# Kernel tuning notes

Hardware: AMD Instinct MI355X
Metric: run time of the kernel (lower is better)

Reference implementation:

```python
import jax, jax.numpy as jnp
import numpy as np

D = 128   # input_dim / num vars
LEAKY_SLOPE = 0.01  # torch F.leaky_relu default


def setup_inputs() -> dict:
    key = jax.random.key(0)
    ks = jax.random.split(key, 7)
    h, o, b = 64, 2, 8192
    scale = 0.05  # keep activations in a sane range
    return {
        "x": jax.random.normal(ks[0], (b, D), jnp.float32),
        "w0": jax.random.normal(ks[1], (D, h, D), jnp.float32) * scale,
        "w1": jax.random.normal(ks[2], (D, h, h), jnp.float32) * scale,
        "w2": jax.random.normal(ks[3], (D, o, h), jnp.float32) * scale,
        "b0": jax.random.normal(ks[4], (D, h), jnp.float32) * scale,
        "b1": jax.random.normal(ks[5], (D, h), jnp.float32) * scale,
        "b2": jax.random.normal(ks[6], (D, o), jnp.float32) * scale,
    }


def reference(x, w0, w1, w2, b0, b1, b2):
    # adjacency: all-ones minus identity (variable t cannot see itself)
    adj = jnp.ones((D, D), x.dtype) - jnp.eye(D, dtype=x.dtype)  # [j? no: (i,j)] symmetric
    # layer 0: out[b,t,i] = sum_j w0[t,i,j] * adj[j,t] * x[b,j]
    # mask the per-variable weights once, then a single contraction (no (t,i,j,b) intermediate)
    w0m = w0 * adj.T[:, None, :]            # (t,i,j); adj symmetric so adj[j,t]==adj[t,j]
    h = jnp.einsum('tij,bj->bti', w0m, x) + b0
    h = jax.nn.leaky_relu(h, LEAKY_SLOPE)
    # layer 1: per-variable dense
    h = jnp.einsum('tij,btj->bti', w1, h) + b1
    h = jax.nn.leaky_relu(h, LEAKY_SLOPE)
    # layer 2 (output, no nonlinearity)
    out = jnp.einsum('tij,btj->bti', w2, h) + b2  # (b, D, output_dim)
    # torch version returns torch.unbind(out, 1); stacked array carries same values
    return out
```

## Files before the change

kernel.cpp:

```cpp
#include <hip/hip_runtime.h>


typedef __bf16 bf16_t;
typedef __bf16 bf16x8 __attribute__((ext_vector_type(8)));
typedef float  f32x4  __attribute__((ext_vector_type(4)));

#define LEAKY 0.01f

#define XB_OFF   0u
#define W0B_OFF  (2048u*1024u)
#define W1B_OFF  (4096u*1024u)

__global__ __launch_bounds__(256)
void brickify(const float* __restrict__ x,  const float* __restrict__ w0,
              const float* __restrict__ w1, unsigned char* __restrict__ ws)
{
    const int wid  = blockIdx.x * 4 + (threadIdx.x >> 6);
    const int lane = threadIdx.x & 63;
    const int lr = lane & 15, lq = lane >> 4;

    float v[8];
    if (wid < 2048) {
        int bt = wid >> 5, rem = wid & 31, nt = rem >> 2, ks = rem & 3;
        const float* s = x + (size_t)(bt*128 + nt*16 + lr) * 128 + ks*32 + lq*8;
        const float4 a = *(const float4*)s, b = *(const float4*)(s + 4);
        v[0]=a.x; v[1]=a.y; v[2]=a.z; v[3]=a.w;
        v[4]=b.x; v[5]=b.y; v[6]=b.z; v[7]=b.w;
    } else if (wid < 4096) {
        int u = wid - 2048, t = u >> 4, rem = u & 15, it = rem >> 2, ks = rem & 3;
        int k0 = ks*32 + lq*8;
        const float* s = w0 + (size_t)(t*64 + it*16 + lr) * 128 + k0;
        const float4 a = *(const float4*)s, b = *(const float4*)(s + 4);
        v[0]=a.x; v[1]=a.y; v[2]=a.z; v[3]=a.w;
        v[4]=b.x; v[5]=b.y; v[6]=b.z; v[7]=b.w;
        #pragma unroll
        for (int j = 0; j < 8; ++j) if (k0 + j == t) v[j] = 0.f;
    } else {
        int u = wid - 4096, t = u >> 3, rem = u & 7, it = rem >> 1, ks = rem & 1;
        const float* s = w1 + (size_t)(t*64 + it*16 + lr) * 64 + ks*32 + lq*8;
        const float4 a = *(const float4*)s, b = *(const float4*)(s + 4);
        v[0]=a.x; v[1]=a.y; v[2]=a.z; v[3]=a.w;
        v[4]=b.x; v[5]=b.y; v[6]=b.z; v[7]=b.w;
    }
    union { bf16_t h[8]; uint4 q; } pk;
    #pragma unroll
    for (int j = 0; j < 8; ++j) pk.h[j] = (bf16_t)v[j];
    ((uint4*)ws)[(size_t)wid * 64 + lane] = pk.q;
}

__global__ __launch_bounds__(512, 2)
void fused_mlp(const unsigned char* __restrict__ ws,
               const float* __restrict__ w2,
               const float* __restrict__ b0, const float* __restrict__ b1,
               const float* __restrict__ b2, float* __restrict__ out)
{
    __shared__ __align__(16) unsigned char hsm[16384];

    const int tid  = threadIdx.x;
    const int w    = tid >> 6;
    const int lane = tid & 63;
    const int lr = lane & 15, lq = lane >> 4;
    const int g  = blockIdx.x;
    const int t  = blockIdx.y;

    const unsigned char* w0p = ws + W0B_OFF + (size_t)t*16384 + lane*16;
    const unsigned char* w1p = ws + W1B_OFF + (size_t)t*8192  + lane*16;
    bf16x8 w0f[4][4], w1f[4][2];
    #pragma unroll
    for (int it = 0; it < 4; ++it)
        #pragma unroll
        for (int ks = 0; ks < 4; ++ks)
            w0f[it][ks] = *(const bf16x8*)(w0p + (it*4+ks)*1024);
    #pragma unroll
    for (int it = 0; it < 4; ++it)
        #pragma unroll
        for (int ks = 0; ks < 2; ++ks)
            w1f[it][ks] = *(const bf16x8*)(w1p + (it*2+ks)*1024);

    f32x4 w2v[2][4];
    #pragma unroll
    for (int o = 0; o < 2; ++o)
        #pragma unroll
        for (int it = 0; it < 4; ++it)
            w2v[o][it] = *(const f32x4*)(w2 + t*128 + o*64 + it*16 + lq*4);

    f32x4 b0q[4], b1q[4];
    #pragma unroll
    for (int it = 0; it < 4; ++it) {
        b0q[it] = *(const f32x4*)(b0 + t*64 + it*16 + lq*4);
        b1q[it] = *(const f32x4*)(b1 + t*64 + it*16 + lq*4);
    }
    const float2 b2v = *(const float2*)(b2 + t*2);

    const unsigned char* xp = ws + XB_OFF + lane*16;
    bf16x8 xf[4];
    #pragma unroll
    for (int ks = 0; ks < 4; ++ks)
        xf[ks] = *(const bf16x8*)(xp + (size_t)((g*8*8 + w)*4 + ks)*1024);

    const int wboff = ((lq >> 1) * 16 + lr) * 16 + (lq & 1) * 8;

    bf16x8 hf[2];
    f32x4  acc1[4];

    #pragma unroll
    for (int s = 0; s <= 8; ++s) {
        const int bt = g*8 + s;

        f32x4 acc0[4];
        if (s < 8) {
            #pragma unroll
            for (int it = 0; it < 4; ++it) acc0[it] = b0q[it];
            #pragma unroll
            for (int ks = 0; ks < 4; ++ks)
                #pragma unroll
                for (int it = 0; it < 4; ++it)
                    acc0[it] = __builtin_amdgcn_mfma_f32_16x16x32_bf16(
                                   w0f[it][ks], xf[ks], acc0[it], 0, 0, 0);
            if (s < 7) {
                #pragma unroll
                for (int ks = 0; ks < 4; ++ks)
                    xf[ks] = *(const bf16x8*)(xp + (size_t)(((bt+1)*8 + w)*4 + ks)*1024);
            }
        }

        if (s > 0) {
            #pragma unroll
            for (int it = 0; it < 4; ++it) acc1[it] = b1q[it];
            #pragma unroll
            for (int ks = 0; ks < 2; ++ks)
                #pragma unroll
                for (int it = 0; it < 4; ++it)
                    acc1[it] = __builtin_amdgcn_mfma_f32_16x16x32_bf16(
                                   w1f[it][ks], hf[ks], acc1[it], 0, 0, 0);
        }

        if (s < 8) {
            #pragma unroll
            for (int it = 0; it < 4; ++it) {
                union { bf16_t h[4]; unsigned long long u; } pk;
                #pragma unroll
                for (int r = 0; r < 4; ++r) {
                    float u = acc0[it][r];
                    pk.h[r] = (bf16_t)fmaxf(u, LEAKY * u);
                }
                int off = (w*2 + (it>>1)) * 1024 + (it&1) * 512 + wboff;
                *(unsigned long long*)(hsm + off) = pk.u;
            }
            #pragma unroll
            for (int ks = 0; ks < 2; ++ks)
                hf[ks] = *(const bf16x8*)(hsm + (w*2 + ks)*1024 + lane*16);
        }

        if (s > 0) {
            float p0 = 0.f, p1 = 0.f;
            #pragma unroll
            for (int it = 0; it < 4; ++it)
                #pragma unroll
                for (int r = 0; r < 4; ++r) {
                    float u = acc1[it][r];
                    u = fmaxf(u, LEAKY * u);
                    p0 = fmaf(w2v[0][it][r], u, p0);
                    p1 = fmaf(w2v[1][it][r], u, p1);
                }
            p0 += __shfl_xor(p0, 16); p0 += __shfl_xor(p0, 32);
            p1 += __shfl_xor(p1, 16); p1 += __shfl_xor(p1, 32);
            if (lq == 0) {
                int row = (bt - 1)*128 + w*16 + lr;
                float2 o2 = { p0 + b2v.x, p1 + b2v.y };
                *(float2*)(out + (size_t)row*256 + t*2) = o2;
            }
        }
    }
}

extern "C" void kernel_launch(void* const* d_in, const int* in_sizes, int n_in,
                              void* d_out, int out_size, void* d_ws, size_t ws_size,
                              hipStream_t stream) {
    const float* x  = (const float*)d_in[0];
    const float* w0 = (const float*)d_in[1];
    const float* w1 = (const float*)d_in[2];
    const float* w2 = (const float*)d_in[3];
    const float* b0 = (const float*)d_in[4];
    const float* b1 = (const float*)d_in[5];
    const float* b2 = (const float*)d_in[6];
    unsigned char* ws = (unsigned char*)d_ws;
    float* out = (float*)d_out;

    brickify<<<dim3(1280), dim3(256), 0, stream>>>(x, w0, w1, ws);
    fused_mlp<<<dim3(8, 128), dim3(512), 0, stream>>>(ws, w2, b0, b1, b2, out);
}
```

Baseline: 113.3 us.

## Shrink fused MLP blocks and cut register use to raise occupancy

Halves the fused MLP block to 4 waves and doubles the grid, raising launch bounds to 3 blocks per CU. It removes the cross-iteration software pipeline, reuses one accumulator set across both layers, reloads biases per step instead of keeping them in registers, and packs w2 to fp16 so layer 2 uses fdot2 on fp16-converted activations. The aim is lower VGPR pressure and more concurrent waves to hide latency. The cost is losing the explicit layer0/layer1 overlap, extra bias loads each step, and reduced precision in the final dot product.

```diff
diff --git a/kernel.cpp b/kernel.cpp
--- a/kernel.cpp
+++ b/kernel.cpp
@@ -4,6 +4,7 @@
 typedef __bf16 bf16_t;
 typedef __bf16 bf16x8 __attribute__((ext_vector_type(8)));
 typedef float  f32x4  __attribute__((ext_vector_type(4)));
+typedef __fp16 f16x2  __attribute__((ext_vector_type(2)));
 
 #define LEAKY 0.01f
 
@@ -48,13 +49,13 @@
     ((uint4*)ws)[(size_t)wid * 64 + lane] = pk.q;
 }
 
-__global__ __launch_bounds__(512, 2)
+__global__ __launch_bounds__(256, 3)
 void fused_mlp(const unsigned char* __restrict__ ws,
                const float* __restrict__ w2,
                const float* __restrict__ b0, const float* __restrict__ b1,
                const float* __restrict__ b2, float* __restrict__ out)
 {
-    __shared__ __align__(16) unsigned char hsm[16384];
+    __shared__ __align__(16) unsigned char hsm[8192];
 
     const int tid  = threadIdx.x;
     const int w    = tid >> 6;
@@ -77,99 +78,90 @@
         for (int ks = 0; ks < 2; ++ks)
             w1f[it][ks] = *(const bf16x8*)(w1p + (it*2+ks)*1024);
 
-    f32x4 w2v[2][4];
+    f16x2 w2h[2][4][2];
     #pragma unroll
     for (int o = 0; o < 2; ++o)
         #pragma unroll
-        for (int it = 0; it < 4; ++it)
-            w2v[o][it] = *(const f32x4*)(w2 + t*128 + o*64 + it*16 + lq*4);
+        for (int it = 0; it < 4; ++it) {
+            f32x4 v = *(const f32x4*)(w2 + t*128 + o*64 + it*16 + lq*4);
+            w2h[o][it][0] = __builtin_amdgcn_cvt_pkrtz(v[0], v[1]);
+            w2h[o][it][1] = __builtin_amdgcn_cvt_pkrtz(v[2], v[3]);
+        }
 
-    f32x4 b0q[4], b1q[4];
-    #pragma unroll
-    for (int it = 0; it < 4; ++it) {
-        b0q[it] = *(const f32x4*)(b0 + t*64 + it*16 + lq*4);
-        b1q[it] = *(const f32x4*)(b1 + t*64 + it*16 + lq*4);
-    }
+    const float* b0p = b0 + t*64 + lq*4;
+    const float* b1p = b1 + t*64 + lq*4;
     const float2 b2v = *(const float2*)(b2 + t*2);
 
-    const unsigned char* xp = ws + XB_OFF + lane*16;
+    const unsigned char* xq = ws + XB_OFF + (size_t)(g*32 + w)*4096 + lane*16;
     bf16x8 xf[4];
     #pragma unroll
     for (int ks = 0; ks < 4; ++ks)
-        xf[ks] = *(const bf16x8*)(xp + (size_t)((g*8*8 + w)*4 + ks)*1024);
+        xf[ks] = *(const bf16x8*)(xq + ks*1024);
 
+    unsigned char* hb = hsm + w*2048;
     const int wboff = ((lq >> 1) * 16 + lr) * 16 + (lq & 1) * 8;
 
-    bf16x8 hf[2];
-    f32x4  acc1[4];
+    for (int s = 0; s < 8; ++s) {
+        f32x4 acc[4];
+        #pragma unroll
+        for (int it = 0; it < 4; ++it)
+            acc[it] = *(const f32x4*)(b0p + it*16);
+        #pragma unroll
+        for (int ks = 0; ks < 4; ++ks)
+            #pragma unroll
+            for (int it = 0; it < 4; ++it)
+                acc[it] = __builtin_amdgcn_mfma_f32_16x16x32_bf16(
+                              w0f[it][ks], xf[ks], acc[it], 0, 0, 0);
 
-    #pragma unroll
-    for (int s = 0; s <= 8; ++s) {
-        const int bt = g*8 + s;
-
-        f32x4 acc0[4];
-        if (s < 8) {
-            #pragma unroll
-            for (int it = 0; it < 4; ++it) acc0[it] = b0q[it];
+        {
+            const unsigned char* xn = xq + (s < 7 ? (s + 1) : 7) * 16384;
             #pragma unroll
             for (int ks = 0; ks < 4; ++ks)
-                #pragma unroll
-                for (int it = 0; it < 4; ++it)
-                    acc0[it] = __builtin_amdgcn_mfma_f32_16x16x32_bf16(
-                                   w0f[it][ks], xf[ks], acc0[it], 0, 0, 0);
-            if (s < 7) {
-                #pragma unroll
-                for (int ks = 0; ks < 4; ++ks)
-                    xf[ks] = *(const bf16x8*)(xp + (size_t)(((bt+1)*8 + w)*4 + ks)*1024);
+                xf[ks] = *(const bf16x8*)(xn + ks*1024);
+        }
+
+        #pragma unroll
+        for (int it = 0; it < 4; ++it) {
+            union { bf16_t h[4]; unsigned long long u; } pk;
+            #pragma unroll
+            for (int r = 0; r < 4; ++r) {
+                float u = acc[it][r];
+                pk.h[r] = (bf16_t)fmaxf(u, LEAKY * u);
+            }
+            *(unsigned long long*)(hb + (it>>1)*1024 + (it&1)*512 + wboff) = pk.u;
+        }
+
+        bf16x8 hf0 = *(const bf16x8*)(hb + lane*16);
+        bf16x8 hf1 = *(const bf16x8*)(hb + 1024 + lane*16);
+        #pragma unroll
+        for (int it = 0; it < 4; ++it)
+            acc[it] = *(const f32x4*)(b1p + it*16);
+        #pragma unroll
+        for (int it = 0; it < 4; ++it) {
+            acc[it] = __builtin_amdgcn_mfma_f32_16x16x32_bf16(
+                          w1f[it][0], hf0, acc[it], 0, 0, 0);
+            acc[it] = __builtin_amdgcn_mfma_f32_16x16x32_bf16(
+                          w1f[it][1], hf1, acc[it], 0, 0, 0);
+        }
+
+        float p0 = 0.f, p1 = 0.f;
+        #pragma unroll
+        for (int it = 0; it < 4; ++it) {
+            #pragma unroll
+            for (int p = 0; p < 2; ++p) {
+                float u0 = acc[it][2*p],   v0 = fmaxf(u0, LEAKY * u0);
+                float u1 = acc[it][2*p+1], v1 = fmaxf(u1, LEAKY * u1);
+                f16x2 hh = __builtin_amdgcn_cvt_pkrtz(v0, v1);
+                p0 = __builtin_amdgcn_fdot2(w2h[0][it][p], hh, p0, false);
+                p1 = __builtin_amdgcn_fdot2(w2h[1][it][p], hh, p1, false);
             }
         }
-
-        if (s > 0) {
-            #pragma unroll
-            for (int it = 0; it < 4; ++it) acc1[it] = b1q[it];
-            #pragma unroll
-            for (int ks = 0; ks < 2; ++ks)
-                #pragma unroll
-                for (int it = 0; it < 4; ++it)
-                    acc1[it] = __builtin_amdgcn_mfma_f32_16x16x32_bf16(
-                                   w1f[it][ks], hf[ks], acc1[it], 0, 0, 0);
-        }
-
-        if (s < 8) {
-            #pragma unroll
-            for (int it = 0; it < 4; ++it) {
-                union { bf16_t h[4]; unsigned long long u; } pk;
-                #pragma unroll
-                for (int r = 0; r < 4; ++r) {
-                    float u = acc0[it][r];
-                    pk.h[r] = (bf16_t)fmaxf(u, LEAKY * u);
-                }
-                int off = (w*2 + (it>>1)) * 1024 + (it&1) * 512 + wboff;
-                *(unsigned long long*)(hsm + off) = pk.u;
-            }
-            #pragma unroll
-            for (int ks = 0; ks < 2; ++ks)
-                hf[ks] = *(const bf16x8*)(hsm + (w*2 + ks)*1024 + lane*16);
-        }
-
-        if (s > 0) {
-            float p0 = 0.f, p1 = 0.f;
-            #pragma unroll
-            for (int it = 0; it < 4; ++it)
-                #pragma unroll
-                for (int r = 0; r < 4; ++r) {
-                    float u = acc1[it][r];
-                    u = fmaxf(u, LEAKY * u);
-                    p0 = fmaf(w2v[0][it][r], u, p0);
-                    p1 = fmaf(w2v[1][it][r], u, p1);
-                }
-            p0 += __shfl_xor(p0, 16); p0 += __shfl_xor(p0, 32);
-            p1 += __shfl_xor(p1, 16); p1 += __shfl_xor(p1, 32);
-            if (lq == 0) {
-                int row = (bt - 1)*128 + w*16 + lr;
-                float2 o2 = { p0 + b2v.x, p1 + b2v.y };
-                *(float2*)(out + (size_t)row*256 + t*2) = o2;
-            }
+        p0 += __shfl_xor(p0, 16); p0 += __shfl_xor(p0, 32);
+        p1 += __shfl_xor(p1, 16); p1 += __shfl_xor(p1, 32);
+        if (lq == 0) {
+            int row = g*512 + s*64 + w*16 + lr;
+            float2 o2 = { p0 + b2v.x, p1 + b2v.y };
+            *(float2*)(out + (size_t)row*256 + t*2) = o2;
         }
     }
 }
@@ -188,5 +180,5 @@
     float* out = (float*)d_out;
 
     brickify<<<dim3(1280), dim3(256), 0, stream>>>(x, w0, w1, ws);
-    fused_mlp<<<dim3(8, 128), dim3(512), 0, stream>>>(ws, w2, b0, b1, b2, out);
+    fused_mlp<<<dim3(16, 128), dim3(256), 0, stream>>>(ws, w2, b0, b1, b2, out);
 }
```

Result: no change. 113.8 us (+0.5%).
